# Kernel tuning notes

Hardware: AMD Instinct MI355X
Metric: run time of the kernel (lower is better)

Reference implementation:

```python
import jax, jax.numpy as jnp
import numpy as np

D_MODEL = 1024
N_HEADS = 16
D_HEAD = D_MODEL // N_HEADS
LUT_SIZE = 4096
TWO_PI = 2.0 * np.pi
SCALE = np.sqrt(2.0 * D_HEAD).astype(np.float32)

# Global sin/cos lookup table over [0, 2*pi), 4096 entries (mirrors get_global_lut(4096)).
_GRID = (TWO_PI * np.arange(LUT_SIZE) / LUT_SIZE).astype(np.float32)
_SIN_TABLE = jnp.asarray(np.sin(_GRID))
_COS_TABLE = jnp.asarray(np.cos(_GRID))


def _lut_sin_cos(theta):
    # quantize angle to nearest LUT bin (wrap mod 2*pi) and gather
    idx = jnp.mod(jnp.round(theta * (LUT_SIZE / TWO_PI)).astype(jnp.int32), LUT_SIZE)
    return _SIN_TABLE[idx], _COS_TABLE[idx]


def setup_inputs() -> dict:
    key = jax.random.key(0)
    ks = jax.random.split(key, 7)
    B, S = 2, 2048
    x = jax.random.normal(ks[0], (B, S, D_MODEL), dtype=jnp.float32)
    w_q = 0.02 * jax.random.normal(ks[1], (N_HEADS, D_HEAD), dtype=jnp.float32)
    b_q = jnp.zeros((N_HEADS, D_HEAD), dtype=jnp.float32)
    w_k = 0.02 * jax.random.normal(ks[2], (N_HEADS, D_HEAD), dtype=jnp.float32)
    b_k = jnp.zeros((N_HEADS, D_HEAD), dtype=jnp.float32)
    v_w = jax.random.normal(ks[3], (D_MODEL, D_MODEL), dtype=jnp.float32) / np.sqrt(D_MODEL)
    out_w = jax.random.normal(ks[4], (D_MODEL, D_MODEL), dtype=jnp.float32) / np.sqrt(D_MODEL)
    return {"x": x, "w_q": w_q, "b_q": b_q, "w_k": w_k, "b_k": b_k, "v_w": v_w, "out_w": out_w}


def reference(x, w_q, b_q, w_k, b_k, v_w, out_w):
    B, S, D = x.shape
    x_heads = x.reshape(B, S, N_HEADS, D_HEAD)

    theta_q = x_heads / (1.0 + jnp.abs(w_q)) + b_q          # (B,S,H,dh)
    sin_q, cos_q = _lut_sin_cos(theta_q)
    Q = jnp.concatenate([cos_q, sin_q], axis=-1)            # (B,S,H,2dh)

    theta_k = x_heads / (1.0 + jnp.abs(w_k)) + b_k
    sin_k, cos_k = _lut_sin_cos(theta_k)
    K = jnp.concatenate([cos_k, sin_k], axis=-1)            # (B,S,H,2dh)

    V = (x @ v_w.T).reshape(B, S, N_HEADS, D_HEAD)          # (B,S,H,dh)

    scores = jnp.einsum("bqhe,bkhe->bhqk", Q, K) / SCALE    # (B,H,S,S)
    causal = jnp.triu(jnp.ones((S, S), dtype=bool), k=1)
    scores = jnp.where(causal, -jnp.inf, scores)
    attn = jax.nn.softmax(scores, axis=-1)

    out = jnp.einsum("bhqk,bkhd->bqhd", attn, V).reshape(B, S, D)
    return out @ out_w.T
```

## Files before the change

### kernel.cpp

```cpp
#include <hip/hip_runtime.h>
#include <hip/hip_bf16.h>
#include <math.h>


typedef __attribute__((ext_vector_type(8))) __bf16 bf16x8;
typedef __attribute__((ext_vector_type(4))) __bf16 bf16x4;
typedef __attribute__((ext_vector_type(4))) float f32x4;
typedef unsigned short ushort_t;
typedef unsigned int uint_t;

#define LUTC 651.8986469044033f
#define ANG 0.0015339807878856412f
#define QSCL 0.12751743590489435f

__device__ __forceinline__ float fast_exp2(float x) {
#if __has_builtin(__builtin_amdgcn_exp2f)
  return __builtin_amdgcn_exp2f(x);
#else
  return exp2f(x);
#endif
}

__device__ __forceinline__ ushort_t f2bf(float f) {
  union { __bf16 b; ushort_t u; } cv;
  cv.b = (__bf16)f;
  return cv.u;
}

__device__ __forceinline__ void store8(ushort_t* p, const ushort_t v[8]) {
  uint4 u;
  u.x = (uint_t)v[0] | ((uint_t)v[1] << 16);
  u.y = (uint_t)v[2] | ((uint_t)v[3] << 16);
  u.z = (uint_t)v[4] | ((uint_t)v[5] << 16);
  u.w = (uint_t)v[6] | ((uint_t)v[7] << 16);
  *(uint4*)p = u;
}

__device__ __forceinline__ void gl_lds16(const void* g, void* l) {
  __builtin_amdgcn_global_load_lds(
      (__attribute__((address_space(1))) void*)(g),
      (__attribute__((address_space(3))) void*)(l),
      16, 0, 0);
}

__global__ __launch_bounds__(256) void prep_kernel(
    const float* __restrict__ x, const float* __restrict__ wq, const float* __restrict__ bq,
    const float* __restrict__ wk, const float* __restrict__ bk,
    ushort_t* __restrict__ Qs, ushort_t* __restrict__ Ks, ushort_t* __restrict__ xb)
{
  int t = blockIdx.x * 256 + threadIdx.x;
  int dm8 = t & 127;
  int g = t >> 7;
  int dm0 = dm8 * 8;
  int h = dm0 >> 6;

  float aq[8], cq[8], ak[8], ck[8];
#pragma unroll
  for (int j = 0; j < 8; ++j) {
    aq[j] = LUTC / (1.0f + fabsf(wq[dm0 + j]));
    cq[j] = LUTC * bq[dm0 + j];
    ak[j] = LUTC / (1.0f + fabsf(wk[dm0 + j]));
    ck[j] = LUTC * bk[dm0 + j];
  }
  for (int i = 0; i < 4; ++i) {
    int bs = g * 4 + i;
    int b = bs >> 11, s = bs & 2047;
    const float4* xp4 = (const float4*)(x + (size_t)bs * 1024 + dm0);
    float4 xa = xp4[0], xbv4 = xp4[1];
    float xv[8] = {xa.x, xa.y, xa.z, xa.w, xbv4.x, xbv4.y, xbv4.z, xbv4.w};
    ushort_t qc[8], qs[8], kc[8], ks[8], xo[8];
#pragma unroll
    for (int j = 0; j < 8; ++j) {
      int iq = ((int)rintf(fmaf(xv[j], aq[j], cq[j]))) & 4095;
      float sq, cqv;
      __sincosf((float)iq * ANG, &sq, &cqv);
      int ik = ((int)rintf(fmaf(xv[j], ak[j], ck[j]))) & 4095;
      float sk, ckv;
      __sincosf((float)ik * ANG, &sk, &ckv);
      qc[j] = f2bf(cqv * QSCL);
      qs[j] = f2bf(sq * QSCL);
      kc[j] = f2bf(ckv);
      ks[j] = f2bf(sk);
      xo[j] = f2bf(xv[j]);
    }
    size_t qb = ((size_t)(b * 16 + h) * 2048 + s) * 128 + (dm0 & 63);
    store8(Qs + qb, qc);        store8(Qs + qb + 64, qs);
    store8(Ks + qb, kc);        store8(Ks + qb + 64, ks);
    store8(xb + (size_t)bs * 1024 + dm0, xo);
  }
}

__global__ __launch_bounds__(256) void wconv_kernel(
    const float* __restrict__ vw, const float* __restrict__ ow,
    ushort_t* __restrict__ vwb, ushort_t* __restrict__ owb)
{
  int t = blockIdx.x * 256 + threadIdx.x;
  const float* src;
  ushort_t* dst;
  int i;
  if (t < 131072) { src = vw; dst = vwb; i = t; }
  else            { src = ow; dst = owb; i = t - 131072; }
  const float4* p4 = (const float4*)(src + (size_t)i * 8);
  float4 a = p4[0], b = p4[1];
  float v[8] = {a.x, a.y, a.z, a.w, b.x, b.y, b.z, b.w};
  ushort_t o[8];
#pragma unroll
  for (int j = 0; j < 8; ++j) o[j] = f2bf(v[j]);
  store8(dst + (size_t)i * 8, o);
}

template <int EPI>
__global__ __launch_bounds__(256) void gemm_nt(
    const ushort_t* __restrict__ A, const ushort_t* __restrict__ B,
    float* __restrict__ Cf, ushort_t* __restrict__ Cb, int M, int N, int K)
{
  __shared__ __align__(16) ushort_t As[128 * 64];
  __shared__ __align__(16) ushort_t Bs[128 * 64];
  const int l = threadIdx.x & 63;
  const int w = threadIdx.x >> 6;
  const int wm = w >> 1, wn = w & 1;
  const int mt = blockIdx.x % (M >> 7);
  const int nt = blockIdx.x / (M >> 7);
  const int m0 = mt << 7, n0 = nt << 7;

  const f32x4 zero4 = {0.f, 0.f, 0.f, 0.f};
  f32x4 acc[4][4];
#pragma unroll
  for (int i = 0; i < 4; ++i)
#pragma unroll
    for (int j = 0; j < 4; ++j) acc[i][j] = zero4;

  for (int k0 = 0; k0 < K; k0 += 64) {
#pragma unroll
    for (int i = 0; i < 4; ++i) {
      int ci = (w * 4 + i) * 64 + l;
      int r = ci >> 3, c = (ci & 7) ^ (r & 7);
      gl_lds16(A + (size_t)(m0 + r) * K + k0 + c * 8, &As[(w * 4 + i) * 512]);
      gl_lds16(B + (size_t)(n0 + r) * K + k0 + c * 8, &Bs[(w * 4 + i) * 512]);
    }
    __syncthreads();
#pragma unroll
    for (int kk = 0; kk < 2; ++kk) {
      bf16x8 af[4], bfr[4];
#pragma unroll
      for (int mi = 0; mi < 4; ++mi) {
        int r = wm * 64 + mi * 16 + (l & 15);
        int ch = ((l >> 4) + 4 * kk) ^ (r & 7);
        af[mi] = *(const bf16x8*)&As[r * 64 + ch * 8];
      }
#pragma unroll
      for (int ni = 0; ni < 4; ++ni) {
        int r = wn * 64 + ni * 16 + (l & 15);
        int ch = ((l >> 4) + 4 * kk) ^ (r & 7);
        bfr[ni] = *(const bf16x8*)&Bs[r * 64 + ch * 8];
      }
#pragma unroll
      for (int mi = 0; mi < 4; ++mi)
#pragma unroll
        for (int ni = 0; ni < 4; ++ni)
          acc[mi][ni] = __builtin_amdgcn_mfma_f32_16x16x32_bf16(af[mi], bfr[ni], acc[mi][ni], 0, 0, 0);
    }
    __syncthreads();
  }

#pragma unroll
  for (int mi = 0; mi < 4; ++mi)
#pragma unroll
    for (int ni = 0; ni < 4; ++ni)
#pragma unroll
      for (int reg = 0; reg < 4; ++reg) {
        int row = m0 + wm * 64 + mi * 16 + (l >> 4) * 4 + reg;
        int col = n0 + wn * 64 + ni * 16 + (l & 15);
        float v = acc[mi][ni][reg];
        if (EPI == 0) {
          Cf[(size_t)row * N + col] = v;
        } else {
          size_t o = (size_t)(col >> 11) * (1024 * 2048) + (size_t)row * 2048 + (col & 2047);
          Cb[o] = f2bf(v);
        }
      }
}


template<bool MASKED>
__device__ __forceinline__ void attn_tile(
    const ushort_t* __restrict__ Kc, const ushort_t* __restrict__ Vc,
    const bf16x8 (&qf)[2][4], f32x4 (&accO)[2][4], f32x4 (&acc_l)[2],
    int kb, int qw, int lo, int g, const bf16x8& ones)
{
  const f32x4 zero4 = {0.f, 0.f, 0.f, 0.f};
  f32x4 sc[2][4];
#pragma unroll
  for (int qm = 0; qm < 2; ++qm)
#pragma unroll
    for (int ns = 0; ns < 4; ++ns) sc[qm][ns] = zero4;

#pragma unroll
  for (int e = 0; e < 4; ++e) {
#pragma unroll
    for (int ns = 0; ns < 4; ++ns) {
      int kr = ns * 16 + lo;
      int cc = (g + 4 * e) ^ (kr & 7);
      bf16x8 kf = *(const bf16x8*)&Kc[kr * 128 + cc * 8];
#pragma unroll
      for (int qm = 0; qm < 2; ++qm)
        sc[qm][ns] = __builtin_amdgcn_mfma_f32_16x16x32_bf16(kf, qf[qm][e], sc[qm][ns], 0, 0, 0);
    }
  }

  bf16x8 pa[2][2];
#pragma unroll
  for (int qm = 0; qm < 2; ++qm) {
#pragma unroll
    for (int ns = 0; ns < 4; ++ns) {
#pragma unroll
      for (int reg = 0; reg < 4; ++reg) {
        float sv = sc[qm][ns][reg];
        if (MASKED) {
          int ka = kb + ns * 16 + g * 4 + reg;
          int qa = qw + qm * 16 + lo;
          sv = (ka <= qa) ? sv : -__builtin_inff();
        }
        pa[qm][ns >> 1][(ns & 1) * 4 + reg] = (__bf16)fast_exp2(sv);
      }
    }
  }

#pragma unroll
  for (int kk = 0; kk < 2; ++kk) {
#pragma unroll
    for (int nd = 0; nd < 4; ++nd) {
      int vr = nd * 16 + lo;
      int h8 = (g & 1) * 4;
      int cc0 = (4 * kk + (g >> 1)) ^ (vr & 7);
      int cc1 = (4 * kk + 2 + (g >> 1)) ^ (vr & 7);
      union { bf16x8 v8; bf16x4 v4[2]; } u;
      u.v4[0] = *(const bf16x4*)&Vc[vr * 64 + cc0 * 8 + h8];
      u.v4[1] = *(const bf16x4*)&Vc[vr * 64 + cc1 * 8 + h8];
#pragma unroll
      for (int qm = 0; qm < 2; ++qm)
        accO[qm][nd] = __builtin_amdgcn_mfma_f32_16x16x32_bf16(pa[qm][kk], u.v8, accO[qm][nd], 0, 0, 0);
    }
#pragma unroll
    for (int qm = 0; qm < 2; ++qm)
      acc_l[qm] = __builtin_amdgcn_mfma_f32_16x16x32_bf16(pa[qm][kk], ones, acc_l[qm], 0, 0, 0);
  }
}

__global__ __launch_bounds__(256) void attn_kernel(
    const ushort_t* __restrict__ Qs, const ushort_t* __restrict__ Ks,
    const ushort_t* __restrict__ Vt, ushort_t* __restrict__ Ob)
{
  const int S = 2048;
  const int id = blockIdx.x;
  const int bh = id & 31;
  const int qt = (id < 256) ? (15 - (id >> 5)) : ((id - 256) >> 5);
  const int l = threadIdx.x & 63;
  const int w = threadIdx.x >> 6;
  const int g = l >> 4, lo = l & 15;

  __shared__ __align__(16) ushort_t Kl[2][64 * 128];
  __shared__ __align__(16) ushort_t Vl[2][64 * 64];

  const int q0b = qt * 128;
  const int qw = q0b + w * 32;
  const ushort_t* Kbase = Ks + (size_t)bh * S * 128;
  const ushort_t* Vbase = Vt + (size_t)bh * 64 * S;

  bf16x8 ones;
#pragma unroll
  for (int j = 0; j < 8; ++j) ones[j] = (__bf16)1.0f;

  bf16x8 qf[2][4];
#pragma unroll
  for (int qm = 0; qm < 2; ++qm) {
    const ushort_t* qp = Qs + ((size_t)bh * S + qw + qm * 16 + lo) * 128 + 8 * g;
#pragma unroll
    for (int e = 0; e < 4; ++e) qf[qm][e] = *(const bf16x8*)(qp + 32 * e);
  }

  const f32x4 zero4 = {0.f, 0.f, 0.f, 0.f};
  f32x4 accO[2][4];
  f32x4 acc_l[2];
#pragma unroll
  for (int qm = 0; qm < 2; ++qm) {
    acc_l[qm] = zero4;
#pragma unroll
    for (int nd = 0; nd < 4; ++nd) accO[qm][nd] = zero4;
  }

  const int nt = 2 * qt + 2;

#define ATTN_STAGE(buf, kb_)                                                    \
  {                                                                             \
    int kb__ = (kb_);                                                           \
    _Pragma("unroll")                                                           \
    for (int i = 0; i < 4; ++i) {                                               \
      int ci = (w * 4 + i) * 64 + l;                                            \
      int r = ci >> 4, c = (ci & 15) ^ (r & 7);                                 \
      gl_lds16(Kbase + (size_t)(kb__ + r) * 128 + c * 8, &Kl[buf][(w * 4 + i) * 512]); \
    }                                                                           \
    _Pragma("unroll")                                                           \
    for (int i = 0; i < 2; ++i) {                                               \
      int ci = (w * 2 + i) * 64 + l;                                            \
      int r = ci >> 3, c = (ci & 7) ^ (r & 7);                                  \
      gl_lds16(Vbase + (size_t)r * S + kb__ + c * 8, &Vl[buf][(w * 2 + i) * 512]); \
    }                                                                           \
  }

  ATTN_STAGE(0, 0);
  ATTN_STAGE(1, 64);
  asm volatile("s_waitcnt vmcnt(6)" ::: "memory");
  __builtin_amdgcn_s_barrier();
  __builtin_amdgcn_sched_barrier(0);

  for (int t = 0; t < nt; ++t) {
    int cb = t & 1;
    if (t < 2 * qt)
      attn_tile<false>(Kl[cb], Vl[cb], qf, accO, acc_l, t * 64, qw, lo, g, ones);
    else
      attn_tile<true>(Kl[cb], Vl[cb], qf, accO, acc_l, t * 64, qw, lo, g, ones);
    __builtin_amdgcn_sched_barrier(0);
    asm volatile("s_waitcnt lgkmcnt(0)" ::: "memory");
    __builtin_amdgcn_s_barrier();
    if (t + 2 < nt) {
      ATTN_STAGE(cb, (t + 2) * 64);
      asm volatile("s_waitcnt vmcnt(6)" ::: "memory");
    } else {
      asm volatile("s_waitcnt vmcnt(0)" ::: "memory");
    }
    __builtin_amdgcn_s_barrier();
    __builtin_amdgcn_sched_barrier(0);
  }
#undef ATTN_STAGE

  float linv[2][4];
#pragma unroll
  for (int qm = 0; qm < 2; ++qm)
#pragma unroll
    for (int reg = 0; reg < 4; ++reg)
      linv[qm][reg] = 1.0f / acc_l[qm][reg];

  const int b = bh >> 4, h = bh & 15;
#pragma unroll
  for (int qm = 0; qm < 2; ++qm)
#pragma unroll
    for (int nd = 0; nd < 4; ++nd)
#pragma unroll
      for (int reg = 0; reg < 4; ++reg) {
        int q = qw + qm * 16 + g * 4 + reg;
        int d = nd * 16 + lo;
        Ob[((size_t)(b * 2048 + q)) * 1024 + h * 64 + d] = f2bf(accO[qm][nd][reg] * linv[qm][reg]);
      }
}

extern "C" void kernel_launch(void* const* d_in, const int* in_sizes, int n_in,
                              void* d_out, int out_size, void* d_ws, size_t ws_size,
                              hipStream_t stream) {
  const float* x  = (const float*)d_in[0];
  const float* wq = (const float*)d_in[1];
  const float* bq = (const float*)d_in[2];
  const float* wk = (const float*)d_in[3];
  const float* bk = (const float*)d_in[4];
  const float* vw = (const float*)d_in[5];
  const float* ow = (const float*)d_in[6];
  float* out = (float*)d_out;

  char* ws = (char*)d_ws;
  ushort_t* Qs  = (ushort_t*)(ws);
  ushort_t* Ksb = (ushort_t*)(ws + (16u << 20));
  ushort_t* Vtb = (ushort_t*)(ws + (32u << 20));
  ushort_t* xbb = (ushort_t*)(ws + (40u << 20));
  ushort_t* Obb = (ushort_t*)(ws + (48u << 20));
  ushort_t* vwb = (ushort_t*)(ws + (56u << 20));
  ushort_t* owb = (ushort_t*)(ws + (58u << 20));

  prep_kernel<<<512, 256, 0, stream>>>(x, wq, bq, wk, bk, Qs, Ksb, xbb);
  wconv_kernel<<<1024, 256, 0, stream>>>(vw, ow, vwb, owb);
  gemm_nt<1><<<256, 256, 0, stream>>>(vwb, xbb, nullptr, Vtb, 1024, 4096, 1024);
  attn_kernel<<<512, 256, 0, stream>>>(Qs, Ksb, Vtb, Obb);
  gemm_nt<0><<<256, 256, 0, stream>>>(Obb, owb, out, nullptr, 4096, 1024, 1024);
}
```

Before: 109.5 us.

## Double-buffer GEMM LDS loads with 64x128 tiles and raise attention priority

The GEMM kernel moves from a 128x128 tile with one LDS buffer to a 64x128 tile with double-buffered LDS stages. Global loads for tile t+2 are issued while tile t is computed, using explicit vmcnt waits and barriers in the same scheme as the attention kernel. The smaller tile doubles the grid to 512 blocks to cover more CUs, at the cost of less reuse per block. The attention loop also raises wave priority with s_setprio around the MFMA tile compute.

Measured after the change: 101.3 us. 1.08x faster.

```diff
diff --git a/kernel.cpp b/kernel.cpp
--- a/kernel.cpp
+++ b/kernel.cpp
@@ -114,63 +114,92 @@
     const ushort_t* __restrict__ A, const ushort_t* __restrict__ B,
     float* __restrict__ Cf, ushort_t* __restrict__ Cb, int M, int N, int K)
 {
-  __shared__ __align__(16) ushort_t As[128 * 64];
-  __shared__ __align__(16) ushort_t Bs[128 * 64];
+  __shared__ __align__(16) ushort_t As[2][64 * 64];
+  __shared__ __align__(16) ushort_t Bs[2][128 * 64];
   const int l = threadIdx.x & 63;
   const int w = threadIdx.x >> 6;
-  const int wm = w >> 1, wn = w & 1;
-  const int mt = blockIdx.x % (M >> 7);
-  const int nt = blockIdx.x / (M >> 7);
-  const int m0 = mt << 7, n0 = nt << 7;
+  const int g = l >> 4, lo = l & 15;
+  const int mt = blockIdx.x % (M >> 6);
+  const int nt = blockIdx.x / (M >> 6);
+  const int m0 = mt << 6, n0 = nt << 7;
 
   const f32x4 zero4 = {0.f, 0.f, 0.f, 0.f};
-  f32x4 acc[4][4];
+  f32x4 acc[4][2];
 #pragma unroll
   for (int i = 0; i < 4; ++i)
 #pragma unroll
-    for (int j = 0; j < 4; ++j) acc[i][j] = zero4;
-
-  for (int k0 = 0; k0 < K; k0 += 64) {
-#pragma unroll
-    for (int i = 0; i < 4; ++i) {
-      int ci = (w * 4 + i) * 64 + l;
-      int r = ci >> 3, c = (ci & 7) ^ (r & 7);
-      gl_lds16(A + (size_t)(m0 + r) * K + k0 + c * 8, &As[(w * 4 + i) * 512]);
-      gl_lds16(B + (size_t)(n0 + r) * K + k0 + c * 8, &Bs[(w * 4 + i) * 512]);
-    }
-    __syncthreads();
+    for (int j = 0; j < 2; ++j) acc[i][j] = zero4;
+
+  const int nk = K >> 6;
+
+#define GEMM_STAGE(buf, k0_)                                                    \
+  {                                                                             \
+    int k0__ = (k0_);                                                           \
+    _Pragma("unroll")                                                           \
+    for (int i = 0; i < 2; ++i) {                                               \
+      int ci = (w * 2 + i) * 64 + l;                                            \
+      int r = ci >> 3, c = (ci & 7) ^ (r & 7);                                  \
+      gl_lds16(A + (size_t)(m0 + r) * K + k0__ + c * 8, &As[buf][(w * 2 + i) * 512]); \
+    }                                                                           \
+    _Pragma("unroll")                                                           \
+    for (int i = 0; i < 4; ++i) {                                               \
+      int ci = (w * 4 + i) * 64 + l;                                            \
+      int r = ci >> 3, c = (ci & 7) ^ (r & 7);                                  \
+      gl_lds16(B + (size_t)(n0 + r) * K + k0__ + c * 8, &Bs[buf][(w * 4 + i) * 512]); \
+    }                                                                           \
+  }
+
+  GEMM_STAGE(0, 0);
+  GEMM_STAGE(1, 64);
+  asm volatile("s_waitcnt vmcnt(6)" ::: "memory");
+  __builtin_amdgcn_s_barrier();
+  __builtin_amdgcn_sched_barrier(0);
+
+  for (int t = 0; t < nk; ++t) {
+    int cb = t & 1;
 #pragma unroll
     for (int kk = 0; kk < 2; ++kk) {
-      bf16x8 af[4], bfr[4];
+      bf16x8 af[4], bfr[2];
 #pragma unroll
       for (int mi = 0; mi < 4; ++mi) {
-        int r = wm * 64 + mi * 16 + (l & 15);
-        int ch = ((l >> 4) + 4 * kk) ^ (r & 7);
-        af[mi] = *(const bf16x8*)&As[r * 64 + ch * 8];
+        int r = mi * 16 + lo;
+        int ch = (g + 4 * kk) ^ (r & 7);
+        af[mi] = *(const bf16x8*)&As[cb][r * 64 + ch * 8];
       }
 #pragma unroll
-      for (int ni = 0; ni < 4; ++ni) {
-        int r = wn * 64 + ni * 16 + (l & 15);
-        int ch = ((l >> 4) + 4 * kk) ^ (r & 7);
-        bfr[ni] = *(const bf16x8*)&Bs[r * 64 + ch * 8];
+      for (int ni = 0; ni < 2; ++ni) {
+        int r = w * 32 + ni * 16 + lo;
+        int ch = (g + 4 * kk) ^ (r & 7);
+        bfr[ni] = *(const bf16x8*)&Bs[cb][r * 64 + ch * 8];
       }
 #pragma unroll
       for (int mi = 0; mi < 4; ++mi)
 #pragma unroll
-        for (int ni = 0; ni < 4; ++ni)
+        for (int ni = 0; ni < 2; ++ni)
           acc[mi][ni] = __builtin_amdgcn_mfma_f32_16x16x32_bf16(af[mi], bfr[ni], acc[mi][ni], 0, 0, 0);
     }
-    __syncthreads();
-  }
+    __builtin_amdgcn_sched_barrier(0);
+    asm volatile("s_waitcnt lgkmcnt(0)" ::: "memory");
+    __builtin_amdgcn_s_barrier();
+    if (t + 2 < nk) {
+      GEMM_STAGE(cb, (t + 2) * 64);
+      asm volatile("s_waitcnt vmcnt(6)" ::: "memory");
+    } else {
+      asm volatile("s_waitcnt vmcnt(0)" ::: "memory");
+    }
+    __builtin_amdgcn_s_barrier();
+    __builtin_amdgcn_sched_barrier(0);
+  }
+#undef GEMM_STAGE
 
 #pragma unroll
   for (int mi = 0; mi < 4; ++mi)
 #pragma unroll
-    for (int ni = 0; ni < 4; ++ni)
+    for (int ni = 0; ni < 2; ++ni)
 #pragma unroll
       for (int reg = 0; reg < 4; ++reg) {
-        int row = m0 + wm * 64 + mi * 16 + (l >> 4) * 4 + reg;
-        int col = n0 + wn * 64 + ni * 16 + (l & 15);
+        int row = m0 + mi * 16 + g * 4 + reg;
+        int col = n0 + w * 32 + ni * 16 + lo;
         float v = acc[mi][ni][reg];
         if (EPI == 0) {
           Cf[(size_t)row * N + col] = v;
@@ -316,10 +345,12 @@
 
   for (int t = 0; t < nt; ++t) {
     int cb = t & 1;
+    __builtin_amdgcn_s_setprio(1);
     if (t < 2 * qt)
       attn_tile<false>(Kl[cb], Vl[cb], qf, accO, acc_l, t * 64, qw, lo, g, ones);
     else
       attn_tile<true>(Kl[cb], Vl[cb], qf, accO, acc_l, t * 64, qw, lo, g, ones);
+    __builtin_amdgcn_s_setprio(0);
     __builtin_amdgcn_sched_barrier(0);
     asm volatile("s_waitcnt lgkmcnt(0)" ::: "memory");
     __builtin_amdgcn_s_barrier();
@@ -377,7 +408,7 @@
 
   prep_kernel<<<512, 256, 0, stream>>>(x, wq, bq, wk, bk, Qs, Ksb, xbb);
   wconv_kernel<<<1024, 256, 0, stream>>>(vw, ow, vwb, owb);
-  gemm_nt<1><<<256, 256, 0, stream>>>(vwb, xbb, nullptr, Vtb, 1024, 4096, 1024);
+  gemm_nt<1><<<512, 256, 0, stream>>>(vwb, xbb, nullptr, Vtb, 1024, 4096, 1024);
   attn_kernel<<<512, 256, 0, stream>>>(Qs, Ksb, Vtb, Obb);
-  gemm_nt<0><<<256, 256, 0, stream>>>(Obb, owb, out, nullptr, 4096, 1024, 1024);
-}
+  gemm_nt<0><<<512, 256, 0, stream>>>(Obb, owb, out, nullptr, 4096, 1024, 1024);
+}
```
